# Performance work log

Measured on AMD Instinct MI355X. Metric: run time of the kernel, lower is better.

Reference implementation:

```python
import jax, jax.numpy as jnp
import numpy as np


def bin_op_s(a, b, w):
    """Differentiable weighted sum over the 16 real-valued binary logic gates.
    a, b: [B, O] soft-boolean inputs; w: [O, 16] gate mixture weights.
    Gate order matches difflogic's bin_op_s.
    """
    ab = a * b
    a_plus_b = a + b
    one = jnp.asarray(1.0, a.dtype)
    # w[:, i] broadcasts [O] against [B, O]
    return (
        # w[:, 0] * 0 (FALSE) contributes nothing
        w[:, 1] * ab                              # a AND b
        + w[:, 2] * (a - ab)                      # a AND NOT b
        + w[:, 3] * a                             # a
        + w[:, 4] * (b - ab)                      # NOT a AND b
        + w[:, 5] * b                             # b
        + w[:, 6] * (a_plus_b - 2.0 * ab)         # a XOR b
        + w[:, 7] * (a_plus_b - ab)               # a OR b
        + w[:, 8] * (one - (a_plus_b - ab))       # NOR
        + w[:, 9] * (one - (a_plus_b - 2.0 * ab)) # XNOR
        + w[:, 10] * (one - b)                    # NOT b
        + w[:, 11] * (one - b + ab)               # b -> a
        + w[:, 12] * (one - a)                    # NOT a
        + w[:, 13] * (one - a + ab)               # a -> b
        + w[:, 14] * (one - ab)                   # NAND
        + w[:, 15] * one                          # TRUE
    )


def setup_inputs() -> dict:
    key = jax.random.key(0)
    k_x, k_w, k_a, k_b = jax.random.split(key, 4)
    B, IN_DIM, OUT_DIM = 2048, 8192, 16384
    x = jax.random.uniform(k_x, (B, IN_DIM), dtype=jnp.float32)
    weights = jax.random.normal(k_w, (OUT_DIM, 16), dtype=jnp.float32)
    idx_a = jax.random.randint(k_a, (OUT_DIM,), 0, IN_DIM, dtype=jnp.int64 if jax.config.jax_enable_x64 else jnp.int32)
    idx_b = jax.random.randint(k_b, (OUT_DIM,), 0, IN_DIM, dtype=jnp.int64 if jax.config.jax_enable_x64 else jnp.int32)
    return {"x": x, "weights": weights, "idx_a": idx_a, "idx_b": idx_b}


def reference(x, weights, idx_a, idx_b):
    # training-mode forward_python: gather the two connected inputs per neuron,
    # softmax the 16 gate logits, and take the soft gate mixture.
    a = x[:, idx_a]  # [B, out_dim]
    b = x[:, idx_b]  # [B, out_dim]
    w = jax.nn.softmax(weights, axis=-1)  # [out_dim, 16]
    return bin_op_s(a, b, w)
```

## Files before the change

kernel.cpp:

```cpp
#include <hip/hip_runtime.h>


#define THREADS 512
#define CTHREADS 256
#define ROWS 2
#define IN_DIM_C 8192

typedef float floatx4 __attribute__((ext_vector_type(4)));

__global__ __launch_bounds__(CTHREADS) void coeffs_k(
    const float* __restrict__ w,
    float* __restrict__ c0o, float* __restrict__ cao,
    float* __restrict__ cbo, float* __restrict__ cabo,
    int OUT_DIM)
{
    const int j = blockIdx.x * CTHREADS + threadIdx.x;
    if (j >= OUT_DIM) return;

    float wv[16];
    const float4* wp = reinterpret_cast<const float4*>(w + (size_t)j * 16);
    #pragma unroll
    for (int q = 0; q < 4; ++q) {
        float4 v = wp[q];
        wv[q * 4 + 0] = v.x; wv[q * 4 + 1] = v.y;
        wv[q * 4 + 2] = v.z; wv[q * 4 + 3] = v.w;
    }

    float m = -1e30f;
    #pragma unroll
    for (int g = 0; g < 16; ++g) m = fmaxf(m, wv[g]);

    float e[16]; float s = 0.f;
    #pragma unroll
    for (int g = 0; g < 16; ++g) { e[g] = __expf(wv[g] - m); s += e[g]; }
    const float inv = 1.f / s;

    const float C0  = e[8] + e[9] + e[10] + e[11] + e[12] + e[13] + e[14] + e[15];
    const float Ca  = e[2] + e[3] + e[6] + e[7] - e[8] - e[9] - e[12] - e[13];
    const float Cb  = e[4] + e[5] + e[6] + e[7] - e[8] - e[9] - e[10] - e[11];
    const float Cab = e[1] - e[2] - e[4] - 2.f * e[6] - e[7]
                    + e[8] + 2.f * e[9] + e[11] + e[13] - e[14];

    c0o[j]  = C0  * inv;
    cao[j]  = Ca  * inv;
    cbo[j]  = Cb  * inv;
    cabo[j] = Cab * inv;
}

__global__ __launch_bounds__(THREADS) void row_k(
    const float* __restrict__ x,
    const float4* __restrict__ c04, const float4* __restrict__ ca4,
    const float4* __restrict__ cb4, const float4* __restrict__ cab4,
    const int4* __restrict__ ia4,
    const int4* __restrict__ ib4,
    float* __restrict__ out,
    int IN_DIM, int OUT_DIM)
{
    __shared__ float2 sx2[IN_DIM_C];

    const int row0 = blockIdx.x * ROWS;
    const int tid  = threadIdx.x;
    const int nchunk = OUT_DIM / (THREADS * 4);

    int4   va = ia4[tid];
    int4   vb = ib4[tid];
    float4 f0 = c04[tid], fa = ca4[tid], fb = cb4[tid], fc = cab4[tid];

    {
        const float4* xr0 = reinterpret_cast<const float4*>(x + (size_t)row0 * IN_DIM);
        const float4* xr1 = reinterpret_cast<const float4*>(x + (size_t)(row0 + 1) * IN_DIM);
        float4* s4 = reinterpret_cast<float4*>(sx2);
        const int n4 = IN_DIM / 4;
        #pragma unroll
        for (int t = tid; t < n4; t += THREADS) {
            const float4 r0 = xr0[t];
            const float4 r1 = xr1[t];
            s4[2 * t + 0] = make_float4(r0.x, r1.x, r0.y, r1.y);
            s4[2 * t + 1] = make_float4(r0.z, r1.z, r0.w, r1.w);
        }
    }
    __syncthreads();

    floatx4* __restrict__ orow0 =
        reinterpret_cast<floatx4*>(out + (size_t)row0 * OUT_DIM);
    floatx4* __restrict__ orow1 =
        reinterpret_cast<floatx4*>(out + (size_t)(row0 + 1) * OUT_DIM);

    #pragma unroll 1
    for (int c = 0; c < nchunk; ++c) {
        const int4   cva = va, cvb = vb;
        const float4 g0 = f0, ga = fa, gb = fb, gc = fc;
        const int j4 = c * THREADS + tid;

        if (c + 1 < nchunk) {
            const int nj4 = j4 + THREADS;
            va = ia4[nj4]; vb = ib4[nj4];
            f0 = c04[nj4]; fa = ca4[nj4]; fb = cb4[nj4]; fc = cab4[nj4];
        }

        const float2 a0 = sx2[cva.x], b0 = sx2[cvb.x];
        const float2 a1 = sx2[cva.y], b1 = sx2[cvb.y];
        const float2 a2 = sx2[cva.z], b2 = sx2[cvb.z];
        const float2 a3 = sx2[cva.w], b3 = sx2[cvb.w];

        floatx4 r0, r1;
        r0.x = fmaf(a0.x * b0.x, gc.x, fmaf(b0.x, gb.x, fmaf(a0.x, ga.x, g0.x)));
        r0.y = fmaf(a1.x * b1.x, gc.y, fmaf(b1.x, gb.y, fmaf(a1.x, ga.y, g0.y)));
        r0.z = fmaf(a2.x * b2.x, gc.z, fmaf(b2.x, gb.z, fmaf(a2.x, ga.z, g0.z)));
        r0.w = fmaf(a3.x * b3.x, gc.w, fmaf(b3.x, gb.w, fmaf(a3.x, ga.w, g0.w)));

        r1.x = fmaf(a0.y * b0.y, gc.x, fmaf(b0.y, gb.x, fmaf(a0.y, ga.x, g0.x)));
        r1.y = fmaf(a1.y * b1.y, gc.y, fmaf(b1.y, gb.y, fmaf(a1.y, ga.y, g0.y)));
        r1.z = fmaf(a2.y * b2.y, gc.z, fmaf(b2.y, gb.z, fmaf(a2.y, ga.z, g0.z)));
        r1.w = fmaf(a3.y * b3.y, gc.w, fmaf(b3.y, gb.w, fmaf(a3.y, ga.w, g0.w)));

        __builtin_nontemporal_store(r0, &orow0[j4]);
        __builtin_nontemporal_store(r1, &orow1[j4]);
    }
}

extern "C" void kernel_launch(void* const* d_in, const int* in_sizes, int n_in,
                              void* d_out, int out_size, void* d_ws, size_t ws_size,
                              hipStream_t stream) {
    const float* x     = (const float*)d_in[0];
    const float* w     = (const float*)d_in[1];
    const int*   idx_a = (const int*)d_in[2];
    const int*   idx_b = (const int*)d_in[3];
    float*       out   = (float*)d_out;

    const int OUT_DIM = in_sizes[2];
    const int B       = out_size / OUT_DIM;
    const int IN_DIM  = in_sizes[0] / B;

    float* c0  = (float*)d_ws;
    float* ca  = c0 + OUT_DIM;
    float* cb  = ca + OUT_DIM;
    float* cab = cb + OUT_DIM;

    coeffs_k<<<(OUT_DIM + CTHREADS - 1) / CTHREADS, CTHREADS, 0, stream>>>(
        w, c0, ca, cb, cab, OUT_DIM);

    row_k<<<B / ROWS, THREADS, 0, stream>>>(
        x,
        reinterpret_cast<const float4*>(c0),
        reinterpret_cast<const float4*>(ca),
        reinterpret_cast<const float4*>(cb),
        reinterpret_cast<const float4*>(cab),
        reinterpret_cast<const int4*>(idx_a),
        reinterpret_cast<const int4*>(idx_b),
        out,
        IN_DIM, OUT_DIM);
}
```

Before: 193.7 us.

## Store x rows as centered fp16 pairs in LDS and pack gather indices

The staged input rows are now held in shared memory as fp16 pairs, shifted by -0.5 to keep precision near the middle of the range, and the gate coefficients are re-expanded to match that shift. This halves LDS usage per block, allowing up to 8 blocks per CU per the launch bounds. The two gather indices are pre-packed into one 32-bit word of byte offsets, cutting index loads. The register prefetch of the next chunk is dropped in favour of relying on occupancy. The risk is reduced accuracy from fp16 storage of inputs.

New measurement: 191.3 us. Within noise of the previous version (-1.3%).

```diff
diff --git a/kernel.cpp b/kernel.cpp
--- a/kernel.cpp
+++ b/kernel.cpp
@@ -1,4 +1,5 @@
 #include <hip/hip_runtime.h>
+#include <hip/hip_fp16.h>
 
 
 #define THREADS 512
@@ -10,8 +11,10 @@
 
 __global__ __launch_bounds__(CTHREADS) void coeffs_k(
     const float* __restrict__ w,
+    const int* __restrict__ ia, const int* __restrict__ ib,
     float* __restrict__ c0o, float* __restrict__ cao,
     float* __restrict__ cbo, float* __restrict__ cabo,
+    unsigned* __restrict__ pko,
     int OUT_DIM)
 {
     const int j = blockIdx.x * CTHREADS + threadIdx.x;
@@ -41,46 +44,61 @@
     const float Cab = e[1] - e[2] - e[4] - 2.f * e[6] - e[7]
                     + e[8] + 2.f * e[9] + e[11] + e[13] - e[14];
 
-    c0o[j]  = C0  * inv;
-    cao[j]  = Ca  * inv;
-    cbo[j]  = Cb  * inv;
+    const float C0s = C0 + 0.5f * (Ca + Cb) + 0.25f * Cab;
+    const float Cas = Ca + 0.5f * Cab;
+    const float Cbs = Cb + 0.5f * Cab;
+
+    c0o[j]  = C0s * inv;
+    cao[j]  = Cas * inv;
+    cbo[j]  = Cbs * inv;
     cabo[j] = Cab * inv;
+
+    const unsigned oa = (unsigned)(ia[j] << 2);
+    const unsigned ob = (unsigned)(ib[j] << 2);
+    pko[j] = oa | (ob << 16);
 }
 
-__global__ __launch_bounds__(THREADS) void row_k(
+__global__ __launch_bounds__(THREADS, 8) void row_k(
     const float* __restrict__ x,
     const float4* __restrict__ c04, const float4* __restrict__ ca4,
     const float4* __restrict__ cb4, const float4* __restrict__ cab4,
-    const int4* __restrict__ ia4,
-    const int4* __restrict__ ib4,
+    const uint4* __restrict__ pk4,
     float* __restrict__ out,
     int IN_DIM, int OUT_DIM)
 {
-    __shared__ float2 sx2[IN_DIM_C];
+    __shared__ __half2 sx[IN_DIM_C];
 
     const int row0 = blockIdx.x * ROWS;
     const int tid  = threadIdx.x;
     const int nchunk = OUT_DIM / (THREADS * 4);
 
-    int4   va = ia4[tid];
-    int4   vb = ib4[tid];
-    float4 f0 = c04[tid], fa = ca4[tid], fb = cb4[tid], fc = cab4[tid];
-
     {
         const float4* xr0 = reinterpret_cast<const float4*>(x + (size_t)row0 * IN_DIM);
         const float4* xr1 = reinterpret_cast<const float4*>(x + (size_t)(row0 + 1) * IN_DIM);
-        float4* s4 = reinterpret_cast<float4*>(sx2);
+        uint4* s4 = reinterpret_cast<uint4*>(sx);
         const int n4 = IN_DIM / 4;
         #pragma unroll
         for (int t = tid; t < n4; t += THREADS) {
             const float4 r0 = xr0[t];
             const float4 r1 = xr1[t];
-            s4[2 * t + 0] = make_float4(r0.x, r1.x, r0.y, r1.y);
-            s4[2 * t + 1] = make_float4(r0.z, r1.z, r0.w, r1.w);
+            const unsigned u0 =
+                (unsigned)__half_as_ushort(__float2half_rn(r0.x - 0.5f)) |
+                ((unsigned)__half_as_ushort(__float2half_rn(r1.x - 0.5f)) << 16);
+            const unsigned u1 =
+                (unsigned)__half_as_ushort(__float2half_rn(r0.y - 0.5f)) |
+                ((unsigned)__half_as_ushort(__float2half_rn(r1.y - 0.5f)) << 16);
+            const unsigned u2 =
+                (unsigned)__half_as_ushort(__float2half_rn(r0.z - 0.5f)) |
+                ((unsigned)__half_as_ushort(__float2half_rn(r1.z - 0.5f)) << 16);
+            const unsigned u3 =
+                (unsigned)__half_as_ushort(__float2half_rn(r0.w - 0.5f)) |
+                ((unsigned)__half_as_ushort(__float2half_rn(r1.w - 0.5f)) << 16);
+            s4[t] = make_uint4(u0, u1, u2, u3);
         }
     }
     __syncthreads();
 
+    const char* sb = reinterpret_cast<const char*>(sx);
     floatx4* __restrict__ orow0 =
         reinterpret_cast<floatx4*>(out + (size_t)row0 * OUT_DIM);
     floatx4* __restrict__ orow1 =
@@ -88,20 +106,24 @@
 
     #pragma unroll 1
     for (int c = 0; c < nchunk; ++c) {
-        const int4   cva = va, cvb = vb;
-        const float4 g0 = f0, ga = fa, gb = fb, gc = fc;
         const int j4 = c * THREADS + tid;
 
-        if (c + 1 < nchunk) {
-            const int nj4 = j4 + THREADS;
-            va = ia4[nj4]; vb = ib4[nj4];
-            f0 = c04[nj4]; fa = ca4[nj4]; fb = cb4[nj4]; fc = cab4[nj4];
-        }
+        const uint4  pk = pk4[j4];
+        const float4 g0 = c04[j4], ga = ca4[j4], gb = cb4[j4], gc = cab4[j4];
 
-        const float2 a0 = sx2[cva.x], b0 = sx2[cvb.x];
-        const float2 a1 = sx2[cva.y], b1 = sx2[cvb.y];
-        const float2 a2 = sx2[cva.z], b2 = sx2[cvb.z];
-        const float2 a3 = sx2[cva.w], b3 = sx2[cvb.w];
+        const __half2 A0 = *reinterpret_cast<const __half2*>(sb + (pk.x & 0xffffu));
+        const __half2 B0 = *reinterpret_cast<const __half2*>(sb + (pk.x >> 16));
+        const __half2 A1 = *reinterpret_cast<const __half2*>(sb + (pk.y & 0xffffu));
+        const __half2 B1 = *reinterpret_cast<const __half2*>(sb + (pk.y >> 16));
+        const __half2 A2 = *reinterpret_cast<const __half2*>(sb + (pk.z & 0xffffu));
+        const __half2 B2 = *reinterpret_cast<const __half2*>(sb + (pk.z >> 16));
+        const __half2 A3 = *reinterpret_cast<const __half2*>(sb + (pk.w & 0xffffu));
+        const __half2 B3 = *reinterpret_cast<const __half2*>(sb + (pk.w >> 16));
+
+        const float2 a0 = __half22float2(A0), b0 = __half22float2(B0);
+        const float2 a1 = __half22float2(A1), b1 = __half22float2(B1);
+        const float2 a2 = __half22float2(A2), b2 = __half22float2(B2);
+        const float2 a3 = __half22float2(A3), b3 = __half22float2(B3);
 
         floatx4 r0, r1;
         r0.x = fmaf(a0.x * b0.x, gc.x, fmaf(b0.x, gb.x, fmaf(a0.x, ga.x, g0.x)));
@@ -132,13 +154,14 @@
     const int B       = out_size / OUT_DIM;
     const int IN_DIM  = in_sizes[0] / B;
 
-    float* c0  = (float*)d_ws;
-    float* ca  = c0 + OUT_DIM;
-    float* cb  = ca + OUT_DIM;
-    float* cab = cb + OUT_DIM;
+    float*    c0  = (float*)d_ws;
+    float*    ca  = c0 + OUT_DIM;
+    float*    cb  = ca + OUT_DIM;
+    float*    cab = cb + OUT_DIM;
+    unsigned* pk  = (unsigned*)(cab + OUT_DIM);
 
     coeffs_k<<<(OUT_DIM + CTHREADS - 1) / CTHREADS, CTHREADS, 0, stream>>>(
-        w, c0, ca, cb, cab, OUT_DIM);
+        w, idx_a, idx_b, c0, ca, cb, cab, pk, OUT_DIM);
 
     row_k<<<B / ROWS, THREADS, 0, stream>>>(
         x,
@@ -146,8 +169,7 @@
         reinterpret_cast<const float4*>(ca),
         reinterpret_cast<const float4*>(cb),
         reinterpret_cast<const float4*>(cab),
-        reinterpret_cast<const int4*>(idx_a),
-        reinterpret_cast<const int4*>(idx_b),
+        reinterpret_cast<const uint4*>(pk),
         out,
         IN_DIM, OUT_DIM);
 }
```
